# Kernel optimization log

Hardware: AMD Instinct MI355X
Metric: run time of the kernel (lower is better)

The kernel has to match this reference:

```python
import jax, jax.numpy as jnp
import numpy as np

B, T, C, H = 4, 2048, 1024, 16
DH = C // H


def setup_inputs() -> dict:
    key = jax.random.key(0)
    k1, k2, k3 = jax.random.split(key, 3)
    x = jax.random.normal(k1, (B, T, C), dtype=jnp.float32)
    w_attn = jax.random.normal(k2, (C, 3 * C), dtype=jnp.float32) * 0.02
    w_proj = jax.random.normal(k3, (C, C), dtype=jnp.float32) * 0.02
    return {"x": x, "w_attn": w_attn, "w_proj": w_proj}


def reference(x, w_attn, w_proj):
    b, t, c = x.shape
    qkv = x @ w_attn  # [B,T,3C]
    q, k, v = jnp.split(qkv, 3, axis=2)
    # [B,T,C] -> [B,H,T,DH]
    q = q.reshape(b, t, H, DH).transpose(0, 2, 1, 3)
    k = k.reshape(b, t, H, DH).transpose(0, 2, 1, 3)
    v = v.reshape(b, t, H, DH).transpose(0, 2, 1, 3)
    scale = 1.0 / np.sqrt(DH).astype(np.float32)
    att = jnp.einsum('bhqd,bhkd->bhqk', q, k) * scale  # [B,H,T,T]
    causal = jnp.tril(jnp.ones((t, t), dtype=bool))
    att = jnp.where(causal[None, None], att, jnp.finfo(att.dtype).min)
    att = jax.nn.softmax(att, axis=-1)
    y = jnp.einsum('bhqk,bhkd->bhqd', att, v)  # [B,H,T,DH]
    y = y.transpose(0, 2, 1, 3).reshape(b, t, c)
    return y @ w_proj
```

## Files before the change

kernel.cpp:

```cpp
#include <hip/hip_runtime.h>
#include <hip/hip_bf16.h>

typedef unsigned short u16;
typedef __attribute__((ext_vector_type(8))) __bf16 bf16x8;
typedef __attribute__((ext_vector_type(4))) float f32x4;
typedef u16 u16x8 __attribute__((ext_vector_type(8)));
typedef u16x8 u16x8a __attribute__((may_alias));
typedef f32x4 f32x4a __attribute__((may_alias));

constexpr int Bz = 4, T = 2048, Cdim = 1024, H = 16, DH = 64;
constexpr int Mrows = Bz * T;
constexpr int N_QKV = 3 * Cdim;
constexpr int Kdim = Cdim;
constexpr float C1 = 0.18033688011118324f;
constexpr float C2 = 34.62468098133512f;

__device__ __forceinline__ u16 f2bf(float f) {
    union { float f; unsigned u; } x; x.f = f;
    if ((x.u & 0x7f800000u) == 0x7f800000u) return 0;
    unsigned r = x.u + 0x7fffu + ((x.u >> 16) & 1u);
    return (u16)(r >> 16);
}

__device__ __forceinline__ bf16x8 as_bf(u16x8 v) {
    union { u16x8 u; bf16x8 b; } x; x.u = v; return x.b;
}

__device__ __forceinline__ void gload_lds16(const u16* g, u16* l) {
    __builtin_amdgcn_global_load_lds(
        (const __attribute__((address_space(1))) void*)g,
        (__attribute__((address_space(3))) void*)l, 16, 0, 0);
}

__global__ __launch_bounds__(256) void cvt_x(
    const float* __restrict__ X, u16* __restrict__ Xb, long n8)
{
    for (long i = blockIdx.x * 256 + threadIdx.x; i < n8; i += (long)gridDim.x * 256) {
        f32x4 a0 = *(const f32x4a*)&X[i * 8];
        f32x4 a1 = *(const f32x4a*)&X[i * 8 + 4];
        u16x8 p;
        p[0] = f2bf(a0[0]); p[1] = f2bf(a0[1]); p[2] = f2bf(a0[2]); p[3] = f2bf(a0[3]);
        p[4] = f2bf(a1[0]); p[5] = f2bf(a1[1]); p[6] = f2bf(a1[2]); p[7] = f2bf(a1[3]);
        *(u16x8a*)&Xb[i * 8] = p;
    }
}

__global__ __launch_bounds__(256) void transpose_cvt(
    const float* __restrict__ W, u16* __restrict__ WT, int K, int N)
{
    const int n = blockIdx.x * 256 + threadIdx.x;
    const int k8 = blockIdx.y * 8;
    u16x8 p;
#pragma unroll
    for (int i = 0; i < 8; ++i) p[i] = f2bf(W[(long)(k8 + i) * N + n]);
    *(u16x8a*)&WT[(long)n * K + k8] = p;
}

template <int MODE>
__global__ __launch_bounds__(256) void gemm_kernel(
    const u16* __restrict__ Ab, const u16* __restrict__ Bw,
    float* __restrict__ out,
    u16* __restrict__ qb, u16* __restrict__ kb, u16* __restrict__ vtb,
    int Nsz, int Ksz)
{
    constexpr int BM = 128, BN = 128, BK = 64;
    __shared__ __align__(16) u16 As[BM * BK];
    __shared__ __align__(16) u16 Bt[BN * BK];

    const int tid = threadIdx.x;
    const int w = tid >> 6, lane = tid & 63, quad = lane >> 4, lr = lane & 15;
    const int wr = (w >> 1) * 64, wc = (w & 1) * 64;
    const int m0 = blockIdx.y * BM, n0 = blockIdx.x * BN;

    const int lrow = lane >> 3;
    const int lcol = (lane & 7) * 8;

    f32x4 acc[4][4] = {};

    for (int k0 = 0; k0 < Ksz; k0 += BK) {
#pragma unroll
        for (int s = 0; s < 4; ++s) {
            const int chunk = w * 4 + s;
            const int r = chunk * 8 + lrow;
            const u16* asrc;
            if (MODE == 1) {
                asrc = &Ab[(long)(m0 + r) * Ksz + k0 + lcol];
            } else {
                const int m = m0 + r, b = m >> 11, t = m & (T - 1), h = k0 >> 6;
                asrc = &Ab[(((long)(b * H + h)) * T + t) * DH + lcol];
            }
            gload_lds16(asrc, &As[chunk * 512]);
            gload_lds16(&Bw[(long)(n0 + r) * Ksz + k0 + lcol], &Bt[chunk * 512]);
        }
        __syncthreads();

#pragma unroll
        for (int ks = 0; ks < 2; ++ks) {
            bf16x8 af[4];
#pragma unroll
            for (int it = 0; it < 4; ++it)
                af[it] = as_bf(*(const u16x8a*)&As[(wr + it * 16 + lr) * BK + ks * 32 + quad * 8]);
#pragma unroll
            for (int jt = 0; jt < 4; ++jt) {
                bf16x8 bfv = as_bf(*(const u16x8a*)&Bt[(wc + jt * 16 + lr) * BK + ks * 32 + quad * 8]);
#pragma unroll
                for (int it = 0; it < 4; ++it)
                    acc[it][jt] = __builtin_amdgcn_mfma_f32_16x16x32_bf16(af[it], bfv, acc[it][jt], 0, 0, 0);
            }
        }
        __syncthreads();
    }

#pragma unroll
    for (int it = 0; it < 4; ++it) {
#pragma unroll
        for (int jt = 0; jt < 4; ++jt) {
#pragma unroll
            for (int r = 0; r < 4; ++r) {
                int m = m0 + wr + it * 16 + quad * 4 + r;
                int n = n0 + wc + jt * 16 + lr;
                if (MODE == 2) {
                    out[(long)m * Nsz + n] = acc[it][jt][r];
                } else {
                    u16 hv = f2bf(acc[it][jt][r]);
                    int b = m >> 11, t = m & (T - 1);
                    int sec = n >> 10, rem = n & 1023, h = rem >> 6, d = rem & 63;
                    int bh = b * H + h;
                    if (sec == 0)      qb [((long)bh * T + t) * DH + d] = hv;
                    else if (sec == 1) kb [((long)bh * T + t) * DH + d] = hv;
                    else               vtb[((long)bh * DH + d) * T + t] = hv;
                }
            }
        }
    }
}

__global__ __launch_bounds__(256) void attn_kernel(
    const u16* qbuf, const u16* __restrict__ kbuf,
    const u16* __restrict__ vtbuf, u16* yb)
{
    constexpr int KS = 72;
    constexpr int PS = 68;
    __shared__ __align__(16) u16 Ks[64 * KS];
    __shared__ __align__(16) u16 Vts[64 * KS];
    __shared__ __align__(16) float Psf[128 * PS];

    const int tid = threadIdx.x;
    const int w = tid >> 6, lane = tid & 63, quad = lane >> 4, lr = lane & 15;
    const int pairi = blockIdx.x;
    const int bh = blockIdx.y;

    const u16* qbase  = qbuf  + (long)bh * T * DH;
    const u16* kbase  = kbuf  + (long)bh * T * DH;
    const u16* vtbase = vtbuf + (long)bh * DH * T;
    u16* ybase = yb + (long)bh * T * DH;

    const int sr0 = tid >> 3;
    const int sc0 = (tid & 7) * 8;

    u16x8 ones_u;
#pragma unroll
    for (int i = 0; i < 8; ++i) ones_u[i] = 0x3F80;
    const bf16x8 onesf = as_bf(ones_u);

    for (int qsel = 0; qsel < 2; ++qsel) {
        const int qblk = qsel ? (15 - pairi) : pairi;
        const int q0 = qblk * 128;

        bf16x8 qf[2][2];
#pragma unroll
        for (int mt = 0; mt < 2; ++mt)
#pragma unroll
            for (int st = 0; st < 2; ++st)
                qf[mt][st] = as_bf(*(const u16x8a*)
                    &qbase[(q0 + w * 32 + mt * 16 + lr) * DH + quad * 8 + st * 32]);

        f32x4 o[2][4] = {};
        f32x4 accl[2] = {};

        const int ktmax = 2 * qblk + 1;

        u16x8 kreg[2], vreg[2];
#pragma unroll
        for (int s = 0; s < 2; ++s) {
            int row = sr0 + s * 32;
            kreg[s] = *(const u16x8a*)&kbase[(long)row * DH + sc0];
            vreg[s] = *(const u16x8a*)&vtbase[(long)row * T + sc0];
        }

        for (int kt = 0; kt <= ktmax; ++kt) {
#pragma unroll
            for (int s = 0; s < 2; ++s) {
                int row = sr0 + s * 32;
                *(u16x8a*)&Ks[row * KS + sc0]  = kreg[s];
                *(u16x8a*)&Vts[row * KS + sc0] = vreg[s];
            }
            __syncthreads();

            if (kt < ktmax) {
#pragma unroll
                for (int s = 0; s < 2; ++s) {
                    int row = sr0 + s * 32;
                    kreg[s] = *(const u16x8a*)&kbase[(long)((kt + 1) * 64 + row) * DH + sc0];
                    vreg[s] = *(const u16x8a*)&vtbase[(long)row * T + (kt + 1) * 64 + sc0];
                }
            }

            f32x4 s_acc[2][4] = {};
#pragma unroll
            for (int st = 0; st < 2; ++st) {
#pragma unroll
                for (int nt = 0; nt < 4; ++nt) {
                    bf16x8 kf = as_bf(*(const u16x8a*)&Ks[(nt * 16 + lr) * KS + quad * 8 + st * 32]);
#pragma unroll
                    for (int mt = 0; mt < 2; ++mt)
                        s_acc[mt][nt] = __builtin_amdgcn_mfma_f32_16x16x32_bf16(
                            qf[mt][st], kf, s_acc[mt][nt], 0, 0, 0);
                }
            }

            if (kt >= 2 * qblk) {
#pragma unroll
                for (int mt = 0; mt < 2; ++mt)
#pragma unroll
                    for (int r = 0; r < 4; ++r) {
                        const int qrow = q0 + w * 32 + mt * 16 + quad * 4 + r;
                        const int prow = (w * 32 + mt * 16 + quad * 4 + r) * PS;
#pragma unroll
                        for (int nt = 0; nt < 4; ++nt) {
                            int key = kt * 64 + nt * 16 + lr;
                            float pv = (key <= qrow)
                                ? __builtin_exp2f(__builtin_fmaf(s_acc[mt][nt][r], C1, -C2))
                                : 0.f;
                            Psf[prow + nt * 16 + lr] = pv;
                        }
                    }
            } else {
#pragma unroll
                for (int mt = 0; mt < 2; ++mt)
#pragma unroll
                    for (int r = 0; r < 4; ++r) {
                        const int prow = (w * 32 + mt * 16 + quad * 4 + r) * PS;
#pragma unroll
                        for (int nt = 0; nt < 4; ++nt)
                            Psf[prow + nt * 16 + lr] =
                                __builtin_exp2f(__builtin_fmaf(s_acc[mt][nt][r], C1, -C2));
                    }
            }
            asm volatile("s_waitcnt lgkmcnt(0)" ::: "memory");

#pragma unroll
            for (int st = 0; st < 2; ++st) {
                bf16x8 pf[2];
#pragma unroll
                for (int mt = 0; mt < 2; ++mt) {
                    const float* pr = &Psf[(w * 32 + mt * 16 + lr) * PS + quad * 8 + st * 32];
                    f32x4 lo = *(const f32x4a*)pr;
                    f32x4 hi = *(const f32x4a*)(pr + 4);
                    union { u16x8 u; unsigned w32[4]; } pk;
                    asm("v_cvt_pk_bf16_f32 %0, %1, %2" : "=v"(pk.w32[0]) : "v"(lo[0]), "v"(lo[1]));
                    asm("v_cvt_pk_bf16_f32 %0, %1, %2" : "=v"(pk.w32[1]) : "v"(lo[2]), "v"(lo[3]));
                    asm("v_cvt_pk_bf16_f32 %0, %1, %2" : "=v"(pk.w32[2]) : "v"(hi[0]), "v"(hi[1]));
                    asm("v_cvt_pk_bf16_f32 %0, %1, %2" : "=v"(pk.w32[3]) : "v"(hi[2]), "v"(hi[3]));
                    pf[mt] = as_bf(pk.u);
                }
#pragma unroll
                for (int mt = 0; mt < 2; ++mt)
                    accl[mt] = __builtin_amdgcn_mfma_f32_16x16x32_bf16(
                        pf[mt], onesf, accl[mt], 0, 0, 0);
#pragma unroll
                for (int dt = 0; dt < 4; ++dt) {
                    bf16x8 vf = as_bf(*(const u16x8a*)&Vts[(dt * 16 + lr) * KS + quad * 8 + st * 32]);
#pragma unroll
                    for (int mt = 0; mt < 2; ++mt)
                        o[mt][dt] = __builtin_amdgcn_mfma_f32_16x16x32_bf16(
                            pf[mt], vf, o[mt][dt], 0, 0, 0);
                }
            }
            __syncthreads();
        }

#pragma unroll
        for (int mt = 0; mt < 2; ++mt) {
#pragma unroll
            for (int dt = 0; dt < 4; ++dt) {
#pragma unroll
                for (int r = 0; r < 4; ++r) {
                    int t = q0 + w * 32 + mt * 16 + quad * 4 + r;
                    int d = dt * 16 + lr;
                    float l = accl[mt][r];
                    float yv = (l > 1e-37f) ? o[mt][dt][r] / l : 0.f;
                    ybase[(long)t * DH + d] = f2bf(yv);
                }
            }
        }
    }
}

extern "C" void kernel_launch(void* const* d_in, const int* in_sizes, int n_in,
                              void* d_out, int out_size, void* d_ws, size_t ws_size,
                              hipStream_t stream) {
    const float* x      = (const float*)d_in[0];
    const float* w_attn = (const float*)d_in[1];
    const float* w_proj = (const float*)d_in[2];
    float* out = (float*)d_out;

    const size_t per = (size_t)Bz * H * T * DH;
    u16* qb  = (u16*)d_ws;
    u16* kb  = qb + per;
    u16* vtb = kb + per;

    u16* xb     = (u16*)d_out;
    u16* watT   = xb + (size_t)Mrows * Kdim;
    u16* wprojT = kb;

    dim3 blk(256);
    cvt_x<<<dim3(2048), blk, 0, stream>>>(x, xb, (long)Mrows * Kdim / 8);
    transpose_cvt<<<dim3(N_QKV / 256, Kdim / 8), blk, 0, stream>>>(
        w_attn, watT, Kdim, N_QKV);
    gemm_kernel<1><<<dim3(N_QKV / 128, Mrows / 128), blk, 0, stream>>>(
        xb, watT, nullptr, qb, kb, vtb, N_QKV, Kdim);
    attn_kernel<<<dim3(8, Bz * H), blk, 0, stream>>>(qb, kb, vtb, qb);
    transpose_cvt<<<dim3(Cdim / 256, Kdim / 8), blk, 0, stream>>>(
        w_proj, wprojT, Kdim, Cdim);
    gemm_kernel<2><<<dim3(Cdim / 128, Mrows / 128), blk, 0, stream>>>(
        qb, wprojT, out, nullptr, nullptr, nullptr, Cdim, Kdim);
}
```

Measured before the change: 292.8 us.

## Double-buffer LDS tiles in GEMM and attention to overlap loads with MFMA

Result: slower. 323.7 us (+10.5%).

```diff
diff --git a/kernel.cpp b/kernel.cpp
--- a/kernel.cpp
+++ b/kernel.cpp
@@ -64,8 +64,8 @@
     int Nsz, int Ksz)
 {
     constexpr int BM = 128, BN = 128, BK = 64;
-    __shared__ __align__(16) u16 As[BM * BK];
-    __shared__ __align__(16) u16 Bt[BN * BK];
+    __shared__ __align__(16) u16 As[2][BM * BK];
+    __shared__ __align__(16) u16 Bt[2][BN * BK];
 
     const int tid = threadIdx.x;
     const int w = tid >> 6, lane = tid & 63, quad = lane >> 4, lr = lane & 15;
@@ -77,7 +77,7 @@
 
     f32x4 acc[4][4] = {};
 
-    for (int k0 = 0; k0 < Ksz; k0 += BK) {
+    auto stage = [&](int buf, int k0) {
 #pragma unroll
         for (int s = 0; s < 4; ++s) {
             const int chunk = w * 4 + s;
@@ -89,27 +89,39 @@
                 const int m = m0 + r, b = m >> 11, t = m & (T - 1), h = k0 >> 6;
                 asrc = &Ab[(((long)(b * H + h)) * T + t) * DH + lcol];
             }
-            gload_lds16(asrc, &As[chunk * 512]);
-            gload_lds16(&Bw[(long)(n0 + r) * Ksz + k0 + lcol], &Bt[chunk * 512]);
-        }
-        __syncthreads();
-
+            gload_lds16(asrc, &As[buf][chunk * 512]);
+            gload_lds16(&Bw[(long)(n0 + r) * Ksz + k0 + lcol], &Bt[buf][chunk * 512]);
+        }
+    };
+
+    auto compute = [&](int buf) {
 #pragma unroll
         for (int ks = 0; ks < 2; ++ks) {
             bf16x8 af[4];
 #pragma unroll
             for (int it = 0; it < 4; ++it)
-                af[it] = as_bf(*(const u16x8a*)&As[(wr + it * 16 + lr) * BK + ks * 32 + quad * 8]);
+                af[it] = as_bf(*(const u16x8a*)&As[buf][(wr + it * 16 + lr) * BK + ks * 32 + quad * 8]);
 #pragma unroll
             for (int jt = 0; jt < 4; ++jt) {
-                bf16x8 bfv = as_bf(*(const u16x8a*)&Bt[(wc + jt * 16 + lr) * BK + ks * 32 + quad * 8]);
+                bf16x8 bfv = as_bf(*(const u16x8a*)&Bt[buf][(wc + jt * 16 + lr) * BK + ks * 32 + quad * 8]);
 #pragma unroll
                 for (int it = 0; it < 4; ++it)
                     acc[it][jt] = __builtin_amdgcn_mfma_f32_16x16x32_bf16(af[it], bfv, acc[it][jt], 0, 0, 0);
             }
         }
+    };
+
+    stage(0, 0);
+    __syncthreads();
+
+    int cur = 0;
+    for (int k0 = 0; k0 < Ksz - BK; k0 += BK) {
+        stage(cur ^ 1, k0 + BK);
+        compute(cur);
         __syncthreads();
+        cur ^= 1;
     }
+    compute(cur);
 
 #pragma unroll
     for (int it = 0; it < 4; ++it) {
@@ -141,8 +153,8 @@
 {
     constexpr int KS = 72;
     constexpr int PS = 68;
-    __shared__ __align__(16) u16 Ks[64 * KS];
-    __shared__ __align__(16) u16 Vts[64 * KS];
+    __shared__ __align__(16) u16 Ks[2][64 * KS];
+    __shared__ __align__(16) u16 Vts[2][64 * KS];
     __shared__ __align__(16) float Psf[128 * PS];
 
     const int tid = threadIdx.x;
@@ -188,12 +200,13 @@
             vreg[s] = *(const u16x8a*)&vtbase[(long)row * T + sc0];
         }
 
+        int cur = 0;
         for (int kt = 0; kt <= ktmax; ++kt) {
 #pragma unroll
             for (int s = 0; s < 2; ++s) {
                 int row = sr0 + s * 32;
-                *(u16x8a*)&Ks[row * KS + sc0]  = kreg[s];
-                *(u16x8a*)&Vts[row * KS + sc0] = vreg[s];
+                *(u16x8a*)&Ks[cur][row * KS + sc0]  = kreg[s];
+                *(u16x8a*)&Vts[cur][row * KS + sc0] = vreg[s];
             }
             __syncthreads();
 
@@ -211,7 +224,7 @@
             for (int st = 0; st < 2; ++st) {
 #pragma unroll
                 for (int nt = 0; nt < 4; ++nt) {
-                    bf16x8 kf = as_bf(*(const u16x8a*)&Ks[(nt * 16 + lr) * KS + quad * 8 + st * 32]);
+                    bf16x8 kf = as_bf(*(const u16x8a*)&Ks[cur][(nt * 16 + lr) * KS + quad * 8 + st * 32]);
 #pragma unroll
                     for (int mt = 0; mt < 2; ++mt)
                         s_acc[mt][nt] = __builtin_amdgcn_mfma_f32_16x16x32_bf16(
@@ -270,14 +283,14 @@
                         pf[mt], onesf, accl[mt], 0, 0, 0);
 #pragma unroll
                 for (int dt = 0; dt < 4; ++dt) {
-                    bf16x8 vf = as_bf(*(const u16x8a*)&Vts[(dt * 16 + lr) * KS + quad * 8 + st * 32]);
+                    bf16x8 vf = as_bf(*(const u16x8a*)&Vts[cur][(dt * 16 + lr) * KS + quad * 8 + st * 32]);
 #pragma unroll
                     for (int mt = 0; mt < 2; ++mt)
                         o[mt][dt] = __builtin_amdgcn_mfma_f32_16x16x32_bf16(
                             pf[mt], vf, o[mt][dt], 0, 0, 0);
                 }
             }
-            __syncthreads();
+            cur ^= 1;
         }
 
 #pragma unroll
```

## Replace QKV GEMM with 256x256 double-buffered, swizzled, phase-scheduled kernel

Applied to the files above, without the earlier changes.

Result: slower. 301.8 us (+3.1%).

```diff
diff --git a/kernel.cpp b/kernel.cpp
--- a/kernel.cpp
+++ b/kernel.cpp
@@ -56,12 +56,151 @@
     *(u16x8a*)&WT[(long)n * K + k8] = p;
 }
 
-template <int MODE>
-__global__ __launch_bounds__(256) void gemm_kernel(
+__global__ __launch_bounds__(512, 2) void gemm_qkv(
     const u16* __restrict__ Ab, const u16* __restrict__ Bw,
-    float* __restrict__ out,
-    u16* __restrict__ qb, u16* __restrict__ kb, u16* __restrict__ vtb,
-    int Nsz, int Ksz)
+    u16* __restrict__ qb, u16* __restrict__ kb, u16* __restrict__ vtb)
+{
+    constexpr int BK = 64, NT = Kdim / BK;
+    __shared__ __align__(16) u16 Asm[2][256 * BK];
+    __shared__ __align__(16) u16 Bsm[2][256 * BK];
+
+    const int tid = threadIdx.x;
+    const int w = tid >> 6, lane = tid & 63, quad = lane >> 4, lr = lane & 15;
+    const int wm = w >> 2, wn = w & 3;
+    const int m0 = blockIdx.y * 256, n0 = blockIdx.x * 256;
+    const int lr7 = lr & 7;
+    const int xsw = (lane & 7) ^ (lane >> 3);
+
+    f32x4 acc[8][4] = {};
+
+    auto stA = [&](int buf, int h, int tile) {
+#pragma unroll
+        for (int c = 0; c < 2; ++c) {
+            const int rb = h * 128 + c * 64 + w * 8;
+            gload_lds16(&Ab[(long)(m0 + rb + (lane >> 3)) * Kdim + tile * BK + xsw * 8],
+                        &Asm[buf][rb * BK]);
+        }
+    };
+    auto stB = [&](int buf, int h, int tile) {
+#pragma unroll
+        for (int c = 0; c < 2; ++c) {
+            const int rb = h * 128 + c * 64 + w * 8;
+            gload_lds16(&Bw[(long)(n0 + rb + (lane >> 3)) * Kdim + tile * BK + xsw * 8],
+                        &Bsm[buf][rb * BK]);
+        }
+    };
+    auto rdA = [&](int buf, int qm, int it, int ks) {
+        const int row = qm * 128 + wm * 64 + it * 16 + lr;
+        return as_bf(*(const u16x8a*)&Asm[buf][row * BK + (((ks * 4 + quad) ^ lr7) * 8)]);
+    };
+    auto rdB = [&](int buf, int qn, int jt, int ks) {
+        const int row = qn * 128 + wn * 32 + jt * 16 + lr;
+        return as_bf(*(const u16x8a*)&Bsm[buf][row * BK + (((ks * 4 + quad) ^ lr7) * 8)]);
+    };
+
+#define MFMA16(QM, QN)                                                          \
+    do {                                                                        \
+        _Pragma("unroll") for (int ks = 0; ks < 2; ++ks)                        \
+        _Pragma("unroll") for (int jt = 0; jt < 2; ++jt)                        \
+        _Pragma("unroll") for (int it = 0; it < 4; ++it)                        \
+            acc[(QM) * 4 + it][(QN) * 2 + jt] =                                 \
+                __builtin_amdgcn_mfma_f32_16x16x32_bf16(                        \
+                    af[it][ks], bf[jt][ks], acc[(QM) * 4 + it][(QN) * 2 + jt],  \
+                    0, 0, 0);                                                   \
+    } while (0)
+
+#define PHASE_TAIL()                                         \
+    asm volatile("s_waitcnt lgkmcnt(0)" ::: "memory");       \
+    __builtin_amdgcn_sched_barrier(0);                       \
+    __builtin_amdgcn_s_setprio(1)
+
+#define PHASE_END()                                          \
+    __builtin_amdgcn_s_setprio(0);                           \
+    asm volatile("" ::: "memory");                           \
+    __builtin_amdgcn_s_barrier();                            \
+    asm volatile("" ::: "memory")
+
+    stA(0, 0, 0); stB(0, 0, 0); stA(0, 1, 0); stB(0, 1, 0);
+    stA(1, 0, 1); stB(1, 0, 1);
+
+    bf16x8 af[4][2], bf[2][2];
+
+    for (int t = 0; t < NT; ++t) {
+        const int buf = t & 1, nbuf = buf ^ 1;
+
+        if (t + 1 < NT) stA(nbuf, 1, t + 1);
+        if (t < NT - 1) asm volatile("s_waitcnt vmcnt(6)" ::: "memory");
+        else            asm volatile("s_waitcnt vmcnt(0)" ::: "memory");
+        __builtin_amdgcn_s_barrier();
+        asm volatile("" ::: "memory");
+#pragma unroll
+        for (int ks = 0; ks < 2; ++ks) {
+#pragma unroll
+            for (int it = 0; it < 4; ++it) af[it][ks] = rdA(buf, 0, it, ks);
+#pragma unroll
+            for (int jt = 0; jt < 2; ++jt) bf[jt][ks] = rdB(buf, 0, jt, ks);
+        }
+        PHASE_TAIL();
+        MFMA16(0, 0);
+        PHASE_END();
+
+#pragma unroll
+        for (int ks = 0; ks < 2; ++ks)
+#pragma unroll
+            for (int jt = 0; jt < 2; ++jt) bf[jt][ks] = rdB(buf, 1, jt, ks);
+        if (t + 1 < NT) stB(nbuf, 1, t + 1);
+        PHASE_TAIL();
+        MFMA16(0, 1);
+        PHASE_END();
+
+#pragma unroll
+        for (int ks = 0; ks < 2; ++ks) {
+#pragma unroll
+            for (int it = 0; it < 4; ++it) af[it][ks] = rdA(buf, 1, it, ks);
+#pragma unroll
+            for (int jt = 0; jt < 2; ++jt) bf[jt][ks] = rdB(buf, 0, jt, ks);
+        }
+        if (t + 2 < NT) stA(buf, 0, t + 2);
+        PHASE_TAIL();
+        MFMA16(1, 0);
+        PHASE_END();
+
+#pragma unroll
+        for (int ks = 0; ks < 2; ++ks)
+#pragma unroll
+            for (int jt = 0; jt < 2; ++jt) bf[jt][ks] = rdB(buf, 1, jt, ks);
+        if (t + 2 < NT) stB(buf, 0, t + 2);
+        PHASE_TAIL();
+        MFMA16(1, 1);
+        PHASE_END();
+    }
+
+#pragma unroll
+    for (int mi = 0; mi < 8; ++mi) {
+#pragma unroll
+        for (int ni = 0; ni < 4; ++ni) {
+#pragma unroll
+            for (int r = 0; r < 4; ++r) {
+                int m = m0 + (mi >> 2) * 128 + wm * 64 + (mi & 3) * 16 + quad * 4 + r;
+                int n = n0 + (ni >> 1) * 128 + wn * 32 + (ni & 1) * 16 + lr;
+                u16 hv = f2bf(acc[mi][ni][r]);
+                int b = m >> 11, tt = m & (T - 1);
+                int sec = n >> 10, rem = n & 1023, h = rem >> 6, d = rem & 63;
+                int bh = b * H + h;
+                if (sec == 0)      qb [((long)bh * T + tt) * DH + d] = hv;
+                else if (sec == 1) kb [((long)bh * T + tt) * DH + d] = hv;
+                else               vtb[((long)bh * DH + d) * T + tt] = hv;
+            }
+        }
+    }
+#undef MFMA16
+#undef PHASE_TAIL
+#undef PHASE_END
+}
+
+__global__ __launch_bounds__(256) void gemm_proj(
+    const u16* __restrict__ Ab, const u16* __restrict__ Bw,
+    float* __restrict__ out, int Nsz, int Ksz)
 {
     constexpr int BM = 128, BN = 128, BK = 64;
     __shared__ __align__(16) u16 As[BM * BK];
@@ -82,14 +221,8 @@
         for (int s = 0; s < 4; ++s) {
             const int chunk = w * 4 + s;
             const int r = chunk * 8 + lrow;
-            const u16* asrc;
-            if (MODE == 1) {
-                asrc = &Ab[(long)(m0 + r) * Ksz + k0 + lcol];
-            } else {
-                const int m = m0 + r, b = m >> 11, t = m & (T - 1), h = k0 >> 6;
-                asrc = &Ab[(((long)(b * H + h)) * T + t) * DH + lcol];
-            }
-            gload_lds16(asrc, &As[chunk * 512]);
+            const int m = m0 + r, b = m >> 11, t = m & (T - 1), h = k0 >> 6;
+            gload_lds16(&Ab[(((long)(b * H + h)) * T + t) * DH + lcol], &As[chunk * 512]);
             gload_lds16(&Bw[(long)(n0 + r) * Ksz + k0 + lcol], &Bt[chunk * 512]);
         }
         __syncthreads();
@@ -112,27 +245,15 @@
     }
 
 #pragma unroll
-    for (int it = 0; it < 4; ++it) {
-#pragma unroll
-        for (int jt = 0; jt < 4; ++jt) {
+    for (int it = 0; it < 4; ++it)
+#pragma unroll
+        for (int jt = 0; jt < 4; ++jt)
 #pragma unroll
             for (int r = 0; r < 4; ++r) {
                 int m = m0 + wr + it * 16 + quad * 4 + r;
                 int n = n0 + wc + jt * 16 + lr;
-                if (MODE == 2) {
-                    out[(long)m * Nsz + n] = acc[it][jt][r];
-                } else {
-                    u16 hv = f2bf(acc[it][jt][r]);
-                    int b = m >> 11, t = m & (T - 1);
-                    int sec = n >> 10, rem = n & 1023, h = rem >> 6, d = rem & 63;
-                    int bh = b * H + h;
-                    if (sec == 0)      qb [((long)bh * T + t) * DH + d] = hv;
-                    else if (sec == 1) kb [((long)bh * T + t) * DH + d] = hv;
-                    else               vtb[((long)bh * DH + d) * T + t] = hv;
-                }
-            }
-        }
-    }
+                out[(long)m * Nsz + n] = acc[it][jt][r];
+            }
 }
 
 __global__ __launch_bounds__(256) void attn_kernel(
@@ -318,11 +439,11 @@
     cvt_x<<<dim3(2048), blk, 0, stream>>>(x, xb, (long)Mrows * Kdim / 8);
     transpose_cvt<<<dim3(N_QKV / 256, Kdim / 8), blk, 0, stream>>>(
         w_attn, watT, Kdim, N_QKV);
-    gemm_kernel<1><<<dim3(N_QKV / 128, Mrows / 128), blk, 0, stream>>>(
-        xb, watT, nullptr, qb, kb, vtb, N_QKV, Kdim);
+    gemm_qkv<<<dim3(N_QKV / 256, Mrows / 256), dim3(512), 0, stream>>>(
+        xb, watT, qb, kb, vtb);
     attn_kernel<<<dim3(8, Bz * H), blk, 0, stream>>>(qb, kb, vtb, qb);
     transpose_cvt<<<dim3(Cdim / 256, Kdim / 8), blk, 0, stream>>>(
         w_proj, wprojT, Kdim, Cdim);
-    gemm_kernel<2><<<dim3(Cdim / 128, Mrows / 128), blk, 0, stream>>>(
-        qb, wprojT, out, nullptr, nullptr, nullptr, Cdim, Kdim);
-}
+    gemm_proj<<<dim3(Cdim / 128, Mrows / 128), blk, 0, stream>>>(
+        qb, wprojT, out, Cdim, Kdim);
+}
```

## Store attention probabilities as bf16 in LDS and split paired query blocks

Applied to the files above, without the earlier changes.

After: 337.5 us. 1.15x slower.

```diff
diff --git a/kernel.cpp b/kernel.cpp
--- a/kernel.cpp
+++ b/kernel.cpp
@@ -140,15 +140,16 @@
     const u16* __restrict__ vtbuf, u16* yb)
 {
     constexpr int KS = 72;
-    constexpr int PS = 68;
     __shared__ __align__(16) u16 Ks[64 * KS];
     __shared__ __align__(16) u16 Vts[64 * KS];
-    __shared__ __align__(16) float Psf[128 * PS];
+    __shared__ __align__(16) u16 Ps[128 * KS];
 
     const int tid = threadIdx.x;
     const int w = tid >> 6, lane = tid & 63, quad = lane >> 4, lr = lane & 15;
-    const int pairi = blockIdx.x;
-    const int bh = blockIdx.y;
+    const int idx = blockIdx.y * 16 + blockIdx.x;
+    const int qblk = idx >> 6;
+    const int bh   = idx & 63;
+    const int q0 = qblk * 128;
 
     const u16* qbase  = qbuf  + (long)bh * T * DH;
     const u16* kbase  = kbuf  + (long)bh * T * DH;
@@ -163,135 +164,119 @@
     for (int i = 0; i < 8; ++i) ones_u[i] = 0x3F80;
     const bf16x8 onesf = as_bf(ones_u);
 
-    for (int qsel = 0; qsel < 2; ++qsel) {
-        const int qblk = qsel ? (15 - pairi) : pairi;
-        const int q0 = qblk * 128;
-
-        bf16x8 qf[2][2];
-#pragma unroll
-        for (int mt = 0; mt < 2; ++mt)
-#pragma unroll
-            for (int st = 0; st < 2; ++st)
-                qf[mt][st] = as_bf(*(const u16x8a*)
-                    &qbase[(q0 + w * 32 + mt * 16 + lr) * DH + quad * 8 + st * 32]);
-
-        f32x4 o[2][4] = {};
-        f32x4 accl[2] = {};
-
-        const int ktmax = 2 * qblk + 1;
-
-        u16x8 kreg[2], vreg[2];
+    bf16x8 qf[2][2];
+#pragma unroll
+    for (int mt = 0; mt < 2; ++mt)
+#pragma unroll
+        for (int st = 0; st < 2; ++st)
+            qf[mt][st] = as_bf(*(const u16x8a*)
+                &qbase[(q0 + w * 32 + mt * 16 + lr) * DH + quad * 8 + st * 32]);
+
+    f32x4 o[2][4] = {};
+    f32x4 accl[2] = {};
+
+    const int ktmax = 2 * qblk + 1;
+
+    u16x8 kreg[2], vreg[2];
+#pragma unroll
+    for (int s = 0; s < 2; ++s) {
+        int row = sr0 + s * 32;
+        kreg[s] = *(const u16x8a*)&kbase[(long)row * DH + sc0];
+        vreg[s] = *(const u16x8a*)&vtbase[(long)row * T + sc0];
+    }
+
+    for (int kt = 0; kt <= ktmax; ++kt) {
 #pragma unroll
         for (int s = 0; s < 2; ++s) {
             int row = sr0 + s * 32;
-            kreg[s] = *(const u16x8a*)&kbase[(long)row * DH + sc0];
-            vreg[s] = *(const u16x8a*)&vtbase[(long)row * T + sc0];
-        }
-
-        for (int kt = 0; kt <= ktmax; ++kt) {
+            *(u16x8a*)&Ks[row * KS + sc0]  = kreg[s];
+            *(u16x8a*)&Vts[row * KS + sc0] = vreg[s];
+        }
+        __syncthreads();
+
+        if (kt < ktmax) {
 #pragma unroll
             for (int s = 0; s < 2; ++s) {
                 int row = sr0 + s * 32;
-                *(u16x8a*)&Ks[row * KS + sc0]  = kreg[s];
-                *(u16x8a*)&Vts[row * KS + sc0] = vreg[s];
-            }
-            __syncthreads();
-
-            if (kt < ktmax) {
-#pragma unroll
-                for (int s = 0; s < 2; ++s) {
-                    int row = sr0 + s * 32;
-                    kreg[s] = *(const u16x8a*)&kbase[(long)((kt + 1) * 64 + row) * DH + sc0];
-                    vreg[s] = *(const u16x8a*)&vtbase[(long)row * T + (kt + 1) * 64 + sc0];
+                kreg[s] = *(const u16x8a*)&kbase[(long)((kt + 1) * 64 + row) * DH + sc0];
+                vreg[s] = *(const u16x8a*)&vtbase[(long)row * T + (kt + 1) * 64 + sc0];
+            }
+        }
+
+        f32x4 s_acc[2][4] = {};
+#pragma unroll
+        for (int st = 0; st < 2; ++st) {
+#pragma unroll
+            for (int nt = 0; nt < 4; ++nt) {
+                bf16x8 kf = as_bf(*(const u16x8a*)&Ks[(nt * 16 + lr) * KS + quad * 8 + st * 32]);
+#pragma unroll
+                for (int mt = 0; mt < 2; ++mt)
+                    s_acc[mt][nt] = __builtin_amdgcn_mfma_f32_16x16x32_bf16(
+                        qf[mt][st], kf, s_acc[mt][nt], 0, 0, 0);
+            }
+        }
+
+        const bool need_mask = (kt >= 2 * qblk);
+#pragma unroll
+        for (int mt = 0; mt < 2; ++mt) {
+#pragma unroll
+            for (int r = 0; r < 4; ++r) {
+                const int qrow = q0 + w * 32 + mt * 16 + quad * 4 + r;
+                const int prow = (w * 32 + mt * 16 + quad * 4 + r) * KS;
+                float pv[4];
+#pragma unroll
+                for (int nt = 0; nt < 4; ++nt) {
+                    float e = __builtin_exp2f(__builtin_fmaf(s_acc[mt][nt][r], C1, -C2));
+                    if (need_mask) {
+                        int key = kt * 64 + nt * 16 + lr;
+                        e = (key <= qrow) ? e : 0.f;
+                    }
+                    pv[nt] = e;
                 }
-            }
-
-            f32x4 s_acc[2][4] = {};
-#pragma unroll
-            for (int st = 0; st < 2; ++st) {
-#pragma unroll
-                for (int nt = 0; nt < 4; ++nt) {
-                    bf16x8 kf = as_bf(*(const u16x8a*)&Ks[(nt * 16 + lr) * KS + quad * 8 + st * 32]);
-#pragma unroll
-                    for (int mt = 0; mt < 2; ++mt)
-                        s_acc[mt][nt] = __builtin_amdgcn_mfma_f32_16x16x32_bf16(
-                            qf[mt][st], kf, s_acc[mt][nt], 0, 0, 0);
-                }
-            }
-
-            if (kt >= 2 * qblk) {
+                unsigned d0, d1;
+                asm("v_cvt_pk_bf16_f32 %0, %1, %2" : "=v"(d0) : "v"(pv[0]), "v"(pv[1]));
+                asm("v_cvt_pk_bf16_f32 %0, %1, %2" : "=v"(d1) : "v"(pv[2]), "v"(pv[3]));
+                Ps[prow +  0 + lr] = (u16)(d0 & 0xffffu);
+                Ps[prow + 16 + lr] = (u16)(d0 >> 16);
+                Ps[prow + 32 + lr] = (u16)(d1 & 0xffffu);
+                Ps[prow + 48 + lr] = (u16)(d1 >> 16);
+            }
+        }
+        asm volatile("s_waitcnt lgkmcnt(0)" ::: "memory");
+
+#pragma unroll
+        for (int st = 0; st < 2; ++st) {
+            bf16x8 pf[2];
+#pragma unroll
+            for (int mt = 0; mt < 2; ++mt)
+                pf[mt] = as_bf(*(const u16x8a*)&Ps[(w * 32 + mt * 16 + lr) * KS + quad * 8 + st * 32]);
+#pragma unroll
+            for (int mt = 0; mt < 2; ++mt)
+                accl[mt] = __builtin_amdgcn_mfma_f32_16x16x32_bf16(
+                    pf[mt], onesf, accl[mt], 0, 0, 0);
+#pragma unroll
+            for (int dt = 0; dt < 4; ++dt) {
+                bf16x8 vf = as_bf(*(const u16x8a*)&Vts[(dt * 16 + lr) * KS + quad * 8 + st * 32]);
 #pragma unroll
                 for (int mt = 0; mt < 2; ++mt)
-#pragma unroll
-                    for (int r = 0; r < 4; ++r) {
-                        const int qrow = q0 + w * 32 + mt * 16 + quad * 4 + r;
-                        const int prow = (w * 32 + mt * 16 + quad * 4 + r) * PS;
-#pragma unroll
-                        for (int nt = 0; nt < 4; ++nt) {
-                            int key = kt * 64 + nt * 16 + lr;
-                            float pv = (key <= qrow)
-                                ? __builtin_exp2f(__builtin_fmaf(s_acc[mt][nt][r], C1, -C2))
-                                : 0.f;
-                            Psf[prow + nt * 16 + lr] = pv;
-                        }
-                    }
-            } else {
-#pragma unroll
-                for (int mt = 0; mt < 2; ++mt)
-#pragma unroll
-                    for (int r = 0; r < 4; ++r) {
-                        const int prow = (w * 32 + mt * 16 + quad * 4 + r) * PS;
-#pragma unroll
-                        for (int nt = 0; nt < 4; ++nt)
-                            Psf[prow + nt * 16 + lr] =
-                                __builtin_exp2f(__builtin_fmaf(s_acc[mt][nt][r], C1, -C2));
-                    }
-            }
-            asm volatile("s_waitcnt lgkmcnt(0)" ::: "memory");
-
-#pragma unroll
-            for (int st = 0; st < 2; ++st) {
-                bf16x8 pf[2];
-#pragma unroll
-                for (int mt = 0; mt < 2; ++mt) {
-                    const float* pr = &Psf[(w * 32 + mt * 16 + lr) * PS + quad * 8 + st * 32];
-                    f32x4 lo = *(const f32x4a*)pr;
-                    f32x4 hi = *(const f32x4a*)(pr + 4);
-                    union { u16x8 u; unsigned w32[4]; } pk;
-                    asm("v_cvt_pk_bf16_f32 %0, %1, %2" : "=v"(pk.w32[0]) : "v"(lo[0]), "v"(lo[1]));
-                    asm("v_cvt_pk_bf16_f32 %0, %1, %2" : "=v"(pk.w32[1]) : "v"(lo[2]), "v"(lo[3]));
-                    asm("v_cvt_pk_bf16_f32 %0, %1, %2" : "=v"(pk.w32[2]) : "v"(hi[0]), "v"(hi[1]));
-                    asm("v_cvt_pk_bf16_f32 %0, %1, %2" : "=v"(pk.w32[3]) : "v"(hi[2]), "v"(hi[3]));
-                    pf[mt] = as_bf(pk.u);
-                }
-#pragma unroll
-                for (int mt = 0; mt < 2; ++mt)
-                    accl[mt] = __builtin_amdgcn_mfma_f32_16x16x32_bf16(
-                        pf[mt], onesf, accl[mt], 0, 0, 0);
-#pragma unroll
-                for (int dt = 0; dt < 4; ++dt) {
-                    bf16x8 vf = as_bf(*(const u16x8a*)&Vts[(dt * 16 + lr) * KS + quad * 8 + st * 32]);
-#pragma unroll
-                    for (int mt = 0; mt < 2; ++mt)
-                        o[mt][dt] = __builtin_amdgcn_mfma_f32_16x16x32_bf16(
-                            pf[mt], vf, o[mt][dt], 0, 0, 0);
-                }
-            }
-            __syncthreads();
-        }
-
-#pragma unroll
-        for (int mt = 0; mt < 2; ++mt) {
-#pragma unroll
-            for (int dt = 0; dt < 4; ++dt) {
-#pragma unroll
-                for (int r = 0; r < 4; ++r) {
-                    int t = q0 + w * 32 + mt * 16 + quad * 4 + r;
-                    int d = dt * 16 + lr;
-                    float l = accl[mt][r];
-                    float yv = (l > 1e-37f) ? o[mt][dt][r] / l : 0.f;
-                    ybase[(long)t * DH + d] = f2bf(yv);
-                }
+                    o[mt][dt] = __builtin_amdgcn_mfma_f32_16x16x32_bf16(
+                        pf[mt], vf, o[mt][dt], 0, 0, 0);
+            }
+        }
+        __syncthreads();
+    }
+
+#pragma unroll
+    for (int mt = 0; mt < 2; ++mt) {
+#pragma unroll
+        for (int dt = 0; dt < 4; ++dt) {
+#pragma unroll
+            for (int r = 0; r < 4; ++r) {
+                int t = q0 + w * 32 + mt * 16 + quad * 4 + r;
+                int d = dt * 16 + lr;
+                float l = accl[mt][r];
+                float yv = (l > 1e-37f) ? o[mt][dt][r] / l : 0.f;
+                ybase[(long)t * DH + d] = f2bf(yv);
             }
         }
     }
@@ -320,7 +305,7 @@
         w_attn, watT, Kdim, N_QKV);
     gemm_kernel<1><<<dim3(N_QKV / 128, Mrows / 128), blk, 0, stream>>>(
         xb, watT, nullptr, qb, kb, vtb, N_QKV, Kdim);
-    attn_kernel<<<dim3(8, Bz * H), blk, 0, stream>>>(qb, kb, vtb, qb);
+    attn_kernel<<<dim3(16, 64), blk, 0, stream>>>(qb, kb, vtb, qb);
     transpose_cvt<<<dim3(Cdim / 256, Kdim / 8), blk, 0, stream>>>(
         w_proj, wprojT, Kdim, Cdim);
     gemm_kernel<2><<<dim3(Cdim / 128, Mrows / 128), blk, 0, stream>>>(
```
